# Performance work log

Measured on AMD Instinct MI355X. Metric: run time of the kernel, lower is better.

The kernel has to match this reference:

```python
import jax, jax.numpy as jnp
import numpy as np

# Device/group constants for group_idx = 0 (from the source)
V_REF = 0.25
G_MIN = 1.0 / 983.3
G_MAX = 1.0 / 281.3
N_AVG = 2.132
N_STD = 0.095

P, N_IN, N_OUT = 1024, 784, 128


def setup_inputs() -> dict:
    key = jax.random.key(0)
    k1, k2, k3, k4, k5, k6 = jax.random.split(key, 6)
    x = jax.random.uniform(k1, (P, N_IN), dtype=jnp.float32)  # normalized pixel-like inputs in [0,1)
    stdv = 1.0 / np.sqrt(N_IN)
    w_pos = 0.5 + stdv * jax.random.normal(k2, (N_IN, N_OUT), dtype=jnp.float32)
    w_neg = 0.5 + stdv * jax.random.normal(k3, (N_IN, N_OUT), dtype=jnp.float32)
    b_pos = 0.5 * jnp.ones((N_OUT,), dtype=jnp.float32)
    b_neg = 0.5 * jnp.ones((N_OUT,), dtype=jnp.float32)
    # per-device nonlinearity parameter n ~ N(n_avg, n_std), crossbar shape (m, 2*n_out)
    n_param = N_AVG + N_STD * jax.random.normal(k4, (N_IN + 1, 2 * N_OUT), dtype=jnp.float32)
    return {"x": x, "w_pos": w_pos, "w_neg": w_neg, "b_pos": b_pos, "b_neg": b_neg, "n_param": n_param}


def reference(x, w_pos, w_neg, b_pos, b_neg, n_param):
    # --- build combined (weights+bias row), pos/neg column-interleaved crossbar params ---
    cw_pos = jnp.concatenate([w_pos, b_pos[None, :]], axis=0)  # (m, n_out), m = n_in+1
    cw_neg = jnp.concatenate([w_neg, b_neg[None, :]], axis=0)  # (m, n_out)
    m = cw_pos.shape[0]
    weights = jnp.stack([cw_pos, cw_neg], axis=-1).reshape(m, -1)  # (m, 2*n_out), interleaved

    max_weight = jnp.max(jnp.abs(weights))
    # w_params_to_G: linear map of nonnegative weight params onto [G_min, G_max]
    G = G_MIN + (G_MAX - G_MIN) * weights / max_weight  # (m, 2n)

    # x_to_V with appended ones column (bias word line)
    k_V = 2.0 * V_REF
    ones = jnp.ones((x.shape[0], 1), dtype=x.dtype)
    inputs = jnp.concatenate([x, ones], axis=1)  # (p, m)
    V = k_V * inputs  # (p, m)

    # nonlinear IV: I(V) = sign(V) * G*V_ref * n ** log2(|V|/V_ref)
    exponent = jnp.log2(jnp.maximum(jnp.abs(V), 1e-12) / V_REF)  # (p, m)
    I_ind = jnp.sign(V)[:, :, None] * (V_REF * G)[None, :, :] * n_param[None, :, :] ** exponent[:, :, None]  # (p, m, 2n)
    I = jnp.sum(I_ind, axis=1)  # bit-line currents, (p, 2n)

    # I_to_y: differential pos-neg columns, undo conductance/voltage scaling
    I_total = I[:, 0::2] - I[:, 1::2]  # (p, n_out)
    y = I_total * (max_weight / (k_V * (G_MAX - G_MIN)))
    return y
```

## Files before the change

kernel.cpp:

```cpp
#include <hip/hip_runtime.h>
#include <hip/hip_bf16.h>

#define P_ROWS   1024
#define N_IN     784
#define N_OUT    128
#define M_ROWS   785
#define OUT_ELEMS (P_ROWS * N_OUT)

#define RATIO_F  ((float)((1.0/983.3) / ((1.0/281.3) - (1.0/983.3))))
#define L_AVG_F  1.0922076f
#define LN2_F    0.6931472f

#define NCHK   12
#define MCH    72
#define KCH    (MCH * 4)
#define NSTEP  (KCH / 32)
#define M_TOT  (NCHK * MCH)
#define NB_MAIN (64 * NCHK)

#define NB_MAX 32

#define PART_MAX_OFF 0
#define CR_OFF       256

typedef _Float16 half8 __attribute__((ext_vector_type(8)));
typedef float    f32x4 __attribute__((ext_vector_type(4)));

__global__ __launch_bounds__(256) void max_reduce_zero(
        const float* __restrict__ wp, const float* __restrict__ wn,
        const float* __restrict__ bp, const float* __restrict__ bn,
        float* __restrict__ partial, float4* __restrict__ out4) {
    const int b = blockIdx.x, t = threadIdx.x;

    const float4 z = make_float4(0.f, 0.f, 0.f, 0.f);
    #pragma unroll
    for (int i = 0; i < 4; ++i)
        out4[(size_t)b * 1024 + i * 256 + t] = z;

    const int nW4 = (N_IN * N_OUT) / 4;
    const float4* wp4 = (const float4*)wp;
    const float4* wn4 = (const float4*)wn;
    int gid = b * 256 + t;
    float v = 0.0f;
    if (gid < N_OUT / 4) {
        float4 a = ((const float4*)bp)[gid], c = ((const float4*)bn)[gid];
        v = fmaxf(fmaxf(fmaxf(fabsf(a.x), fabsf(a.y)), fmaxf(fabsf(a.z), fabsf(a.w))),
                  fmaxf(fmaxf(fabsf(c.x), fabsf(c.y)), fmaxf(fabsf(c.z), fabsf(c.w))));
    }
    for (int i = gid; i < nW4; i += NB_MAX * 256) {
        float4 a = wp4[i], c = wn4[i];
        v = fmaxf(v, fmaxf(fmaxf(fabsf(a.x), fabsf(a.y)), fmaxf(fabsf(a.z), fabsf(a.w))));
        v = fmaxf(v, fmaxf(fmaxf(fabsf(c.x), fabsf(c.y)), fmaxf(fabsf(c.z), fabsf(c.w))));
    }
    for (int off = 32; off > 0; off >>= 1)
        v = fmaxf(v, __shfl_down(v, off, 64));
    __shared__ float smax[4];
    if ((t & 63) == 0) smax[t >> 6] = v;
    __syncthreads();
    if (t == 0)
        partial[b] = fmaxf(fmaxf(smax[0], smax[1]), fmaxf(smax[2], smax[3]));
}

__global__ __launch_bounds__(256) void precompute_c(
        const float* __restrict__ wp, const float* __restrict__ wn,
        const float* __restrict__ bp, const float* __restrict__ bn,
        const float* __restrict__ np, const float* __restrict__ partial,
        _Float16* __restrict__ Cr) {
    float mw = 0.0f;
    #pragma unroll
    for (int i = 0; i < NB_MAX; ++i) mw = fmaxf(mw, partial[i]);
    const float c0 = 0.5f * RATIO_F * mw;

    int idx = blockIdx.x * 256 + threadIdx.x;
    int m = idx >> 7, n = idx & 127;
    float C0 = 0.f, C1 = 0.f, C2 = 0.f, C3 = 0.f;
    if (m < M_ROWS) {
        float wpv = (m < N_IN) ? wp[m * N_OUT + n] : bp[n];
        float wnv = (m < N_IN) ? wn[m * N_OUT + n] : bn[n];
        float npv = np[m * (2 * N_OUT) + 2 * n];
        float nnv = np[m * (2 * N_OUT) + 2 * n + 1];
        float Dp = LN2_F * (__builtin_amdgcn_logf(npv) - L_AVG_F);
        float Dn = LN2_F * (__builtin_amdgcn_logf(nnv) - L_AVG_F);
        float Ap = c0 + 0.5f * wpv;
        float An = c0 + 0.5f * wnv;
        float ApD = Ap * Dp,    AnD = An * Dn;
        float ApD2 = ApD * Dp,  AnD2 = AnD * Dn;
        float ApD3 = ApD2 * Dp, AnD3 = AnD2 * Dn;
        C0 = Ap - An;
        C1 = ApD - AnD;
        C2 = (ApD2 - AnD2) * 0.5f;
        C3 = (ApD3 - AnD3) * (1.0f / 6.0f);
    }
    const int c  = m / MCH;
    const int ml = m - c * MCH;
    const int s  = ml >> 3;
    const int q  = (ml >> 1) & 3;
    const int h  = (ml & 1) * 4;
    _Float16* dst = Cr + (((((size_t)c * NSTEP + s) * 4 + q) * 128 + n) * 8 + h);
    dst[0] = (_Float16)C0;
    dst[1] = (_Float16)C1;
    dst[2] = (_Float16)C2;
    dst[3] = (_Float16)C3;
}

__global__ __launch_bounds__(256) void memristor_main(
        const float* __restrict__ x, const _Float16* __restrict__ Cr,
        float* __restrict__ out) {
    const int bid = blockIdx.x;
    const int ch  = bid % NCHK;
    const int pb  = bid / NCHK;
    const int p0  = pb * 16;
    const int m0  = ch * MCH;
    const int t   = threadIdx.x;

    __shared__ half8 F_lds[36 * 16];
    const int NF4 = MCH / 4;
    for (int idx = t; idx < 16 * NF4; idx += 256) {
        const int p     = idx / NF4;
        const int f4    = idx - p * NF4;
        const int mbase = m0 + f4 * 4;
        float xv[4];
        if (mbase + 3 < N_IN) {
            float4 v = *(const float4*)(x + (size_t)(p0 + p) * N_IN + mbase);
            xv[0] = v.x; xv[1] = v.y; xv[2] = v.z; xv[3] = v.w;
        } else {
            #pragma unroll
            for (int u = 0; u < 4; ++u) {
                int m = mbase + u;
                xv[u] = (m < N_IN) ? x[(size_t)(p0 + p) * N_IN + m] : -1.0f;
            }
        }
        #pragma unroll
        for (int u = 0; u < 4; ++u) {
            const int m  = mbase + u;
            const int ml = m - m0;
            float e;
            if (m < N_IN)
                e = (xv[u] > 0.0f) ? __builtin_amdgcn_logf(2.0f * xv[u]) : -1.0e4f;
            else
                e = (m == N_IN) ? 1.0f : -1.0e4f;
            float F0 = __builtin_amdgcn_exp2f(e * L_AVG_F);
            float F1 = F0 * e, F2 = F1 * e, F3 = F2 * e;
            _Float16* dst = (_Float16*)&F_lds[(ml >> 1) * 16 + p] + (ml & 1) * 4;
            dst[0] = (_Float16)F0;
            dst[1] = (_Float16)F1;
            dst[2] = (_Float16)F2;
            dst[3] = (_Float16)F3;
        }
    }
    __syncthreads();

    const int lane = t & 63;
    const int w    = t >> 6;
    const int quad = lane >> 4;
    const int col  = lane & 15;
    const int n0   = w * 32;

    const _Float16* __restrict__ Bb = Cr + (size_t)ch * (NSTEP * 4 * 128 * 8);

    f32x4 acc0 = {0.f, 0.f, 0.f, 0.f};
    f32x4 acc1 = {0.f, 0.f, 0.f, 0.f};
    #pragma unroll
    for (int s = 0; s < NSTEP; ++s) {
        half8 a  = F_lds[(s * 4 + quad) * 16 + col];
        half8 b0 = *(const half8*)(Bb + (((s * 4 + quad) * 128) + n0 + col) * 8);
        half8 b1 = *(const half8*)(Bb + (((s * 4 + quad) * 128) + n0 + 16 + col) * 8);
        acc0 = __builtin_amdgcn_mfma_f32_16x16x32_f16(a, b0, acc0, 0, 0, 0);
        acc1 = __builtin_amdgcn_mfma_f32_16x16x32_f16(a, b1, acc1, 0, 0, 0);
    }

    float* obase = out + (size_t)(p0 + quad * 4) * N_OUT;
    #pragma unroll
    for (int r = 0; r < 4; ++r) {
        unsafeAtomicAdd(&obase[(size_t)r * N_OUT + n0 + col],      acc0[r]);
        unsafeAtomicAdd(&obase[(size_t)r * N_OUT + n0 + 16 + col], acc1[r]);
    }
}

extern "C" void kernel_launch(void* const* d_in, const int* in_sizes, int n_in,
                              void* d_out, int out_size, void* d_ws, size_t ws_size,
                              hipStream_t stream) {
    const float* x  = (const float*)d_in[0];
    const float* wp = (const float*)d_in[1];
    const float* wn = (const float*)d_in[2];
    const float* bp = (const float*)d_in[3];
    const float* bn = (const float*)d_in[4];
    const float* np = (const float*)d_in[5];
    float* out = (float*)d_out;

    float*     partial = (float*)((char*)d_ws + PART_MAX_OFF);
    _Float16*  Cr      = (_Float16*)((char*)d_ws + CR_OFF);

    max_reduce_zero<<<NB_MAX, 256, 0, stream>>>(wp, wn, bp, bn, partial, (float4*)out);
    precompute_c<<<(M_TOT * 128) / 256, 256, 0, stream>>>(wp, wn, bp, bn, np, partial, Cr);
    memristor_main<<<NB_MAIN, 256, 0, stream>>>(x, Cr, out);
}
```

Measured before the change: 76.51 us.

## Fuse coefficient precompute into main MFMA kernel, recomputing B on the fly

Removes the separate precompute kernel and its fp16 workspace; each main block now derives its polynomial coefficients from weights and n_param directly before the MFMAs. The aim is to eliminate one launch and a global round-trip. In exchange, the log-based coefficient work is repeated by every row block, and strided fp32 loads are used. Chunk count is reduced to 11 with bias handled specially in the last step, and the max-reduce grid is widened.

```diff
diff --git a/kernel.cpp b/kernel.cpp
--- a/kernel.cpp
+++ b/kernel.cpp
@@ -5,23 +5,17 @@
 #define N_IN     784
 #define N_OUT    128
 #define M_ROWS   785
-#define OUT_ELEMS (P_ROWS * N_OUT)
 
 #define RATIO_F  ((float)((1.0/983.3) / ((1.0/281.3) - (1.0/983.3))))
 #define L_AVG_F  1.0922076f
 #define LN2_F    0.6931472f
 
-#define NCHK   12
+#define NCHK   11
 #define MCH    72
-#define KCH    (MCH * 4)
-#define NSTEP  (KCH / 32)
-#define M_TOT  (NCHK * MCH)
+#define NSTEP  9
 #define NB_MAIN (64 * NCHK)
 
-#define NB_MAX 32
-
-#define PART_MAX_OFF 0
-#define CR_OFF       256
+#define NB_MAX 64
 
 typedef _Float16 half8 __attribute__((ext_vector_type(8)));
 typedef float    f32x4 __attribute__((ext_vector_type(4)));
@@ -34,8 +28,8 @@
 
     const float4 z = make_float4(0.f, 0.f, 0.f, 0.f);
     #pragma unroll
-    for (int i = 0; i < 4; ++i)
-        out4[(size_t)b * 1024 + i * 256 + t] = z;
+    for (int i = 0; i < 2; ++i)
+        out4[(size_t)b * 512 + i * 256 + t] = z;
 
     const int nW4 = (N_IN * N_OUT) / 4;
     const float4* wp4 = (const float4*)wp;
@@ -61,50 +55,49 @@
         partial[b] = fmaxf(fmaxf(smax[0], smax[1]), fmaxf(smax[2], smax[3]));
 }
 
-__global__ __launch_bounds__(256) void precompute_c(
+__device__ __forceinline__ void genB(int m, int n, float c0,
+        const float* __restrict__ wp, const float* __restrict__ wn,
+        const float* __restrict__ npar, float C[4]) {
+    float wpv = wp[(size_t)m * N_OUT + n];
+    float wnv = wn[(size_t)m * N_OUT + n];
+    float2 nv = *(const float2*)(npar + (size_t)m * (2 * N_OUT) + 2 * n);
+    float Dp = LN2_F * (__builtin_amdgcn_logf(nv.x) - L_AVG_F);
+    float Dn = LN2_F * (__builtin_amdgcn_logf(nv.y) - L_AVG_F);
+    float Ap = c0 + 0.5f * wpv;
+    float An = c0 + 0.5f * wnv;
+    float ApD = Ap * Dp,    AnD = An * Dn;
+    float ApD2 = ApD * Dp,  AnD2 = AnD * Dn;
+    float ApD3 = ApD2 * Dp, AnD3 = AnD2 * Dn;
+    C[0] = Ap - An;
+    C[1] = ApD - AnD;
+    C[2] = (ApD2 - AnD2) * 0.5f;
+    C[3] = (ApD3 - AnD3) * (1.0f / 6.0f);
+}
+
+__device__ __forceinline__ void genBias(int n, float c0,
+        const float* __restrict__ bp, const float* __restrict__ bn,
+        const float* __restrict__ npar, float C[4]) {
+    float wpv = bp[n];
+    float wnv = bn[n];
+    float2 nv = *(const float2*)(npar + (size_t)N_IN * (2 * N_OUT) + 2 * n);
+    float Dp = LN2_F * (__builtin_amdgcn_logf(nv.x) - L_AVG_F);
+    float Dn = LN2_F * (__builtin_amdgcn_logf(nv.y) - L_AVG_F);
+    float Ap = c0 + 0.5f * wpv;
+    float An = c0 + 0.5f * wnv;
+    float ApD = Ap * Dp,    AnD = An * Dn;
+    float ApD2 = ApD * Dp,  AnD2 = AnD * Dn;
+    float ApD3 = ApD2 * Dp, AnD3 = AnD2 * Dn;
+    C[0] = Ap - An;
+    C[1] = ApD - AnD;
+    C[2] = (ApD2 - AnD2) * 0.5f;
+    C[3] = (ApD3 - AnD3) * (1.0f / 6.0f);
+}
+
+__global__ __launch_bounds__(256, 3) void memristor_main(
+        const float* __restrict__ x,
         const float* __restrict__ wp, const float* __restrict__ wn,
         const float* __restrict__ bp, const float* __restrict__ bn,
-        const float* __restrict__ np, const float* __restrict__ partial,
-        _Float16* __restrict__ Cr) {
-    float mw = 0.0f;
-    #pragma unroll
-    for (int i = 0; i < NB_MAX; ++i) mw = fmaxf(mw, partial[i]);
-    const float c0 = 0.5f * RATIO_F * mw;
-
-    int idx = blockIdx.x * 256 + threadIdx.x;
-    int m = idx >> 7, n = idx & 127;
-    float C0 = 0.f, C1 = 0.f, C2 = 0.f, C3 = 0.f;
-    if (m < M_ROWS) {
-        float wpv = (m < N_IN) ? wp[m * N_OUT + n] : bp[n];
-        float wnv = (m < N_IN) ? wn[m * N_OUT + n] : bn[n];
-        float npv = np[m * (2 * N_OUT) + 2 * n];
-        float nnv = np[m * (2 * N_OUT) + 2 * n + 1];
-        float Dp = LN2_F * (__builtin_amdgcn_logf(npv) - L_AVG_F);
-        float Dn = LN2_F * (__builtin_amdgcn_logf(nnv) - L_AVG_F);
-        float Ap = c0 + 0.5f * wpv;
-        float An = c0 + 0.5f * wnv;
-        float ApD = Ap * Dp,    AnD = An * Dn;
-        float ApD2 = ApD * Dp,  AnD2 = AnD * Dn;
-        float ApD3 = ApD2 * Dp, AnD3 = AnD2 * Dn;
-        C0 = Ap - An;
-        C1 = ApD - AnD;
-        C2 = (ApD2 - AnD2) * 0.5f;
-        C3 = (ApD3 - AnD3) * (1.0f / 6.0f);
-    }
-    const int c  = m / MCH;
-    const int ml = m - c * MCH;
-    const int s  = ml >> 3;
-    const int q  = (ml >> 1) & 3;
-    const int h  = (ml & 1) * 4;
-    _Float16* dst = Cr + (((((size_t)c * NSTEP + s) * 4 + q) * 128 + n) * 8 + h);
-    dst[0] = (_Float16)C0;
-    dst[1] = (_Float16)C1;
-    dst[2] = (_Float16)C2;
-    dst[3] = (_Float16)C3;
-}
-
-__global__ __launch_bounds__(256) void memristor_main(
-        const float* __restrict__ x, const _Float16* __restrict__ Cr,
+        const float* __restrict__ npar, const float* __restrict__ partial,
         float* __restrict__ out) {
     const int bid = blockIdx.x;
     const int ch  = bid % NCHK;
@@ -112,6 +105,11 @@
     const int p0  = pb * 16;
     const int m0  = ch * MCH;
     const int t   = threadIdx.x;
+
+    float mw = 0.0f;
+    #pragma unroll
+    for (int i = 0; i < NB_MAX; ++i) mw = fmaxf(mw, partial[i]);
+    const float c0 = 0.5f * RATIO_F * mw;
 
     __shared__ half8 F_lds[36 * 16];
     const int NF4 = MCH / 4;
@@ -155,16 +153,43 @@
     const int quad = lane >> 4;
     const int col  = lane & 15;
     const int n0   = w * 32;
-
-    const _Float16* __restrict__ Bb = Cr + (size_t)ch * (NSTEP * 4 * 128 * 8);
+    const int nA   = n0 + col;
+    const int nB   = n0 + 16 + col;
+    const int mq   = m0 + quad * 2;
 
     f32x4 acc0 = {0.f, 0.f, 0.f, 0.f};
     f32x4 acc1 = {0.f, 0.f, 0.f, 0.f};
     #pragma unroll
     for (int s = 0; s < NSTEP; ++s) {
-        half8 a  = F_lds[(s * 4 + quad) * 16 + col];
-        half8 b0 = *(const half8*)(Bb + (((s * 4 + quad) * 128) + n0 + col) * 8);
-        half8 b1 = *(const half8*)(Bb + (((s * 4 + quad) * 128) + n0 + 16 + col) * 8);
+        half8 a = F_lds[(s * 4 + quad) * 16 + col];
+        half8 b0, b1;
+        if (s < 8 || ch != NCHK - 1) {
+            #pragma unroll
+            for (int bb = 0; bb < 2; ++bb) {
+                const int m = mq + s * 8 + bb;
+                float CA[4], CB[4];
+                genB(m, nA, c0, wp, wn, npar, CA);
+                genB(m, nB, c0, wp, wn, npar, CB);
+                #pragma unroll
+                for (int j = 0; j < 4; ++j) {
+                    b0[bb * 4 + j] = (_Float16)CA[j];
+                    b1[bb * 4 + j] = (_Float16)CB[j];
+                }
+            }
+        } else {
+            #pragma unroll
+            for (int j = 0; j < 8; ++j) { b0[j] = (_Float16)0.f; b1[j] = (_Float16)0.f; }
+            if (quad == 0) {
+                float CA[4], CB[4];
+                genBias(nA, c0, bp, bn, npar, CA);
+                genBias(nB, c0, bp, bn, npar, CB);
+                #pragma unroll
+                for (int j = 0; j < 4; ++j) {
+                    b0[j] = (_Float16)CA[j];
+                    b1[j] = (_Float16)CB[j];
+                }
+            }
+        }
         acc0 = __builtin_amdgcn_mfma_f32_16x16x32_f16(a, b0, acc0, 0, 0, 0);
         acc1 = __builtin_amdgcn_mfma_f32_16x16x32_f16(a, b1, acc1, 0, 0, 0);
     }
@@ -188,10 +213,8 @@
     const float* np = (const float*)d_in[5];
     float* out = (float*)d_out;
 
-    float*     partial = (float*)((char*)d_ws + PART_MAX_OFF);
-    _Float16*  Cr      = (_Float16*)((char*)d_ws + CR_OFF);
+    float* partial = (float*)d_ws;
 
     max_reduce_zero<<<NB_MAX, 256, 0, stream>>>(wp, wn, bp, bn, partial, (float4*)out);
-    precompute_c<<<(M_TOT * 128) / 256, 256, 0, stream>>>(wp, wn, bp, bn, np, partial, Cr);
-    memristor_main<<<NB_MAIN, 256, 0, stream>>>(x, Cr, out);
-}
+    memristor_main<<<NB_MAIN, 256, 0, stream>>>(x, wp, wn, bp, bn, np, partial, out);
+}
```

New measurement: 77.24 us. Within noise of the previous version (+1.0%).
